# Performance work log

Hardware: AMD Instinct MI355X
Metric: run time of the kernel (lower is better)

## Reference

```python
import jax, jax.numpy as jnp
import numpy as np

B, L, E, H = 4, 2048, 1024, 16
D = E // H  # per-head dim

def setup_inputs() -> dict:
    key = jax.random.key(0)
    ks = jax.random.split(key, 12)
    xav = lambda k, shape: jax.random.normal(k, shape, jnp.float32) * (2.0 / (shape[0] + shape[-1])) ** 0.5
    embeddings = jax.random.normal(ks[0], (B, L, E), jnp.float32)
    pre_proj_w = xav(ks[1], (E, E)); pre_proj_b = jnp.zeros((E,), jnp.float32)
    pre_sparse_w = xav(ks[2], (E, E)); pre_sparse_b = jnp.zeros((E,), jnp.float32)
    toeplitz_psfs = xav(ks[3], (H, 2 * L - 1, D))
    post_conv_w = xav(ks[4], (E, E)); post_conv_b = jnp.zeros((E,), jnp.float32)
    dens = 0.01
    num_nz = int(L * L * dens)
    idxs = jax.random.randint(ks[5], (num_nz, 2), 0, L)
    vals = jnp.abs(jax.random.normal(ks[6], (num_nz,), jnp.float32))
    sparse = jnp.zeros((L, L), jnp.float32).at[idxs[:, 0], idxs[:, 1]].add(vals)
    ln_gamma = jnp.ones((E,), jnp.float32); ln_beta = jnp.zeros((E,), jnp.float32)
    return {"embeddings": embeddings, "pre_proj_w": pre_proj_w, "pre_proj_b": pre_proj_b,
            "pre_sparse_w": pre_sparse_w, "pre_sparse_b": pre_sparse_b,
            "toeplitz_psfs": toeplitz_psfs, "post_conv_w": post_conv_w, "post_conv_b": post_conv_b,
            "sparse": sparse, "ln_gamma": ln_gamma, "ln_beta": ln_beta}

def reference(embeddings, pre_proj_w, pre_proj_b, pre_sparse_w, pre_sparse_b,
              toeplitz_psfs, post_conv_w, post_conv_b, sparse, ln_gamma, ln_beta):
    b, l, e = embeddings.shape
    h, two_l_m1, d = toeplitz_psfs.shape
    # causal PSF mask: first l taps kept, trailing l-1 zeroed (before softmax)
    psf_mask = jnp.concatenate([jnp.ones((l,)), jnp.zeros((l - 1,))])[None, :, None]
    psfs = jax.nn.softmax(toeplitz_psfs * psf_mask, axis=1)  # softmax over 2l-1 taps
    # pre-projection
    pre = jnp.einsum('ble,oe->blo', embeddings, pre_proj_w) + pre_proj_b
    # pad seq to 2l-1 and split heads: [b, h, 2l-1, d]
    padded = jnp.pad(pre, ((0, 0), (0, l - 1), (0, 0)))
    padded = padded.reshape(b, two_l_m1, h, d).transpose(0, 2, 1, 3)
    # 2D FFT convolution over (seq, per-head-dim)
    psf_fft = jnp.fft.fftn(psfs, axes=(1, 2))              # [h, 2l-1, d]
    emb_fft = jnp.fft.fftn(padded, axes=(2, 3))            # [b, h, 2l-1, d]
    conv = jnp.real(jnp.fft.ifftn(psf_fft[None] * emb_fft, axes=(2, 3)))[:, :, :l, :]
    conv = jax.nn.gelu(conv, approximate=False)
    conv = conv.transpose(0, 2, 1, 3).reshape(b, l, e)
    conv_emb = jnp.einsum('ble,oe->blo', conv, post_conv_w) + post_conv_b
    # sparse branch (causal lower-triangular mask)
    sparse_masked = sparse * jnp.tril(jnp.ones((l, l), sparse.dtype))
    pre_sparse = jnp.einsum('ble,oe->blo', pre, pre_sparse_w) + pre_sparse_b
    sparse_emb = jnp.einsum('ls,bse->ble', sparse_masked, pre_sparse)
    # residual + layernorm (dropout = identity at eval)
    x = conv_emb + sparse_emb + embeddings
    mu = jnp.mean(x, axis=-1, keepdims=True)
    var = jnp.mean(jnp.square(x - mu), axis=-1, keepdims=True)
    return (x - mu) * jax.lax.rsqrt(var + 1e-12) * ln_gamma + ln_beta
```

## Files before the change

kernel.cpp:

```cpp
#include <hip/hip_runtime.h>
#include <hip/hip_bf16.h>
#include <hip/hip_fp16.h>
#include <math.h>

#define B_ 4
#define L_ 2048
#define E_ 1024
#define H_ 16
#define D_ 64
#define NFFT 4096
#define CAP 128

typedef __hip_bfloat16 bf16;
typedef __attribute__((ext_vector_type(8))) short bf16x8;
typedef __attribute__((ext_vector_type(4))) float f32x4;
typedef __attribute__((ext_vector_type(2))) __fp16 f16x2;

typedef __attribute__((address_space(1))) const unsigned int gas_u32;
typedef __attribute__((address_space(3))) unsigned int las_u32;

__device__ __forceinline__ void gload_lds16(const void* g, void* l) {
    __builtin_amdgcn_global_load_lds((gas_u32*)g, (las_u32*)l, 16, 0, 0);
}

#define SL(i) ((i) + ((i) >> 4))
#define LDSN (NFFT + NFFT / 16)

__device__ __forceinline__ float bfu2f(unsigned short u) {
    return __uint_as_float(((unsigned)u) << 16);
}
__device__ __forceinline__ f16x2 pk2(float a, float b) {
    return __builtin_amdgcn_cvt_pkrtz(a, b);
}

__device__ __forceinline__ int drev64(int k) {
    return ((k & 3) << 4) | (k & 12) | ((k >> 4) & 3);
}

#define C1R 0.923879532511287f
#define C1I -0.382683432365090f
#define C2R 0.707106781186548f
#define C2I -0.707106781186548f
#define C3R 0.382683432365090f
#define C3I -0.923879532511287f

__device__ __forceinline__ void r4dif_w(float& x0r, float& x0i, float& x1r, float& x1i,
                                        float& x2r, float& x2i, float& x3r, float& x3i,
                                        float w1r, float w1i) {
    float a0r = x0r + x2r, a0i = x0i + x2i, a1r = x0r - x2r, a1i = x0i - x2i;
    float a2r = x1r + x3r, a2i = x1i + x3i, a3r = x1r - x3r, a3i = x1i - x3i;
    float y0r = a0r + a2r, y0i = a0i + a2i, y2r = a0r - a2r, y2i = a0i - a2i;
    float y1r = a1r + a3i, y1i = a1i - a3r, y3r = a1r - a3i, y3i = a1i + a3r;
    float w2r = w1r * w1r - w1i * w1i, w2i = 2.0f * w1r * w1i;
    float w3r = w2r * w1r - w2i * w1i, w3i = w2r * w1i + w2i * w1r;
    x0r = y0r; x0i = y0i;
    x1r = y1r * w1r - y1i * w1i; x1i = y1r * w1i + y1i * w1r;
    x2r = y2r * w2r - y2i * w2i; x2i = y2r * w2i + y2i * w2r;
    x3r = y3r * w3r - y3i * w3i; x3i = y3r * w3i + y3i * w3r;
}
__device__ __forceinline__ void r4dif_nt(float& x0r, float& x0i, float& x1r, float& x1i,
                                         float& x2r, float& x2i, float& x3r, float& x3i) {
    float a0r = x0r + x2r, a0i = x0i + x2i, a1r = x0r - x2r, a1i = x0i - x2i;
    float a2r = x1r + x3r, a2i = x1i + x3i, a3r = x1r - x3r, a3i = x1i - x3i;
    x0r = a0r + a2r; x0i = a0i + a2i;
    x2r = a0r - a2r; x2i = a0i - a2i;
    float y1r = a1r + a3i, y1i = a1i - a3r, y3r = a1r - a3i, y3i = a1i + a3r;
    x1r = y1r; x1i = y1i; x3r = y3r; x3i = y3i;
}
__device__ __forceinline__ void r4dit_w(float& x0r, float& x0i, float& x1r, float& x1i,
                                        float& x2r, float& x2i, float& x3r, float& x3i,
                                        float w1r, float w1i) {
    float w2r = w1r * w1r - w1i * w1i, w2i = 2.0f * w1r * w1i;
    float w3r = w2r * w1r - w2i * w1i, w3i = w2r * w1i + w2i * w1r;
    float z1r = x1r * w1r + x1i * w1i, z1i = x1i * w1r - x1r * w1i;
    float z2r = x2r * w2r + x2i * w2i, z2i = x2i * w2r - x2r * w2i;
    float z3r = x3r * w3r + x3i * w3i, z3i = x3i * w3r - x3r * w3i;
    float b0r = x0r + z2r, b0i = x0i + z2i, b1r = x0r - z2r, b1i = x0i - z2i;
    float b2r = z1r + z3r, b2i = z1i + z3i, b3r = z1r - z3r, b3i = z1i - z3i;
    x0r = b0r + b2r; x0i = b0i + b2i;
    x2r = b0r - b2r; x2i = b0i - b2i;
    x1r = b1r - b3i; x1i = b1i + b3r;
    x3r = b1r + b3i; x3i = b1i - b3r;
}
__device__ __forceinline__ void r4dit_nt(float& x0r, float& x0i, float& x1r, float& x1i,
                                         float& x2r, float& x2i, float& x3r, float& x3i) {
    float b0r = x0r + x2r, b0i = x0i + x2i, b1r = x0r - x2r, b1i = x0i - x2i;
    float b2r = x1r + x3r, b2i = x1i + x3i, b3r = x1r - x3r, b3i = x1i - x3i;
    x0r = b0r + b2r; x0i = b0i + b2i;
    x2r = b0r - b2r; x2i = b0i - b2i;
    x1r = b1r - b3i; x1i = b1i + b3r;
    x3r = b1r + b3i; x3i = b1i - b3r;
}

__device__ __forceinline__ void fftA_fwd(float* xr, float* xi, float wpr, float wpi) {
    r4dif_w(xr[0], xi[0], xr[4], xi[4], xr[8], xi[8], xr[12], xi[12], wpr, wpi);
    r4dif_w(xr[1], xi[1], xr[5], xi[5], xr[9], xi[9], xr[13], xi[13],
            wpr * C1R - wpi * C1I, wpr * C1I + wpi * C1R);
    r4dif_w(xr[2], xi[2], xr[6], xi[6], xr[10], xi[10], xr[14], xi[14],
            wpr * C2R - wpi * C2I, wpr * C2I + wpi * C2R);
    r4dif_w(xr[3], xi[3], xr[7], xi[7], xr[11], xi[11], xr[15], xi[15],
            wpr * C3R - wpi * C3I, wpr * C3I + wpi * C3R);
    float s2r = wpr * wpr - wpi * wpi, s2i = 2.0f * wpr * wpi;
    float w4r = s2r * s2r - s2i * s2i, w4i = 2.0f * s2r * s2i;
#pragma unroll
    for (int g = 0; g < 4; ++g)
        r4dif_w(xr[4 * g], xi[4 * g], xr[4 * g + 1], xi[4 * g + 1], xr[4 * g + 2],
                xi[4 * g + 2], xr[4 * g + 3], xi[4 * g + 3], w4r, w4i);
}
__device__ __forceinline__ void fftA_inv(float* xr, float* xi, float wpr, float wpi) {
    float s2r = wpr * wpr - wpi * wpi, s2i = 2.0f * wpr * wpi;
    float w4r = s2r * s2r - s2i * s2i, w4i = 2.0f * s2r * s2i;
#pragma unroll
    for (int g = 0; g < 4; ++g)
        r4dit_w(xr[4 * g], xi[4 * g], xr[4 * g + 1], xi[4 * g + 1], xr[4 * g + 2],
                xi[4 * g + 2], xr[4 * g + 3], xi[4 * g + 3], w4r, w4i);
    r4dit_w(xr[0], xi[0], xr[4], xi[4], xr[8], xi[8], xr[12], xi[12], wpr, wpi);
    r4dit_w(xr[1], xi[1], xr[5], xi[5], xr[9], xi[9], xr[13], xi[13],
            wpr * C1R - wpi * C1I, wpr * C1I + wpi * C1R);
    r4dit_w(xr[2], xi[2], xr[6], xi[6], xr[10], xi[10], xr[14], xi[14],
            wpr * C2R - wpi * C2I, wpr * C2I + wpi * C2R);
    r4dit_w(xr[3], xi[3], xr[7], xi[7], xr[11], xi[11], xr[15], xi[15],
            wpr * C3R - wpi * C3I, wpr * C3I + wpi * C3R);
}
__device__ __forceinline__ void fftB_fwd(float* xr, float* xi, float wor, float woi) {
    r4dif_w(xr[0], xi[0], xr[4], xi[4], xr[8], xi[8], xr[12], xi[12], wor, woi);
    r4dif_w(xr[1], xi[1], xr[5], xi[5], xr[9], xi[9], xr[13], xi[13],
            wor * C1R - woi * C1I, wor * C1I + woi * C1R);
    r4dif_w(xr[2], xi[2], xr[6], xi[6], xr[10], xi[10], xr[14], xi[14],
            wor * C2R - woi * C2I, wor * C2I + woi * C2R);
    r4dif_w(xr[3], xi[3], xr[7], xi[7], xr[11], xi[11], xr[15], xi[15],
            wor * C3R - woi * C3I, wor * C3I + woi * C3R);
    float s2r = wor * wor - woi * woi, s2i = 2.0f * wor * woi;
    float w4r = s2r * s2r - s2i * s2i, w4i = 2.0f * s2r * s2i;
#pragma unroll
    for (int g = 0; g < 4; ++g)
        r4dif_w(xr[4 * g], xi[4 * g], xr[4 * g + 1], xi[4 * g + 1], xr[4 * g + 2],
                xi[4 * g + 2], xr[4 * g + 3], xi[4 * g + 3], w4r, w4i);
}
__device__ __forceinline__ void fftB_inv(float* xr, float* xi, float wor, float woi) {
    float s2r = wor * wor - woi * woi, s2i = 2.0f * wor * woi;
    float w4r = s2r * s2r - s2i * s2i, w4i = 2.0f * s2r * s2i;
#pragma unroll
    for (int g = 0; g < 4; ++g)
        r4dit_w(xr[4 * g], xi[4 * g], xr[4 * g + 1], xi[4 * g + 1], xr[4 * g + 2],
                xi[4 * g + 2], xr[4 * g + 3], xi[4 * g + 3], w4r, w4i);
    r4dit_w(xr[0], xi[0], xr[4], xi[4], xr[8], xi[8], xr[12], xi[12], wor, woi);
    r4dit_w(xr[1], xi[1], xr[5], xi[5], xr[9], xi[9], xr[13], xi[13],
            wor * C1R - woi * C1I, wor * C1I + woi * C1R);
    r4dit_w(xr[2], xi[2], xr[6], xi[6], xr[10], xi[10], xr[14], xi[14],
            wor * C2R - woi * C2I, wor * C2I + woi * C2R);
    r4dit_w(xr[3], xi[3], xr[7], xi[7], xr[11], xi[11], xr[15], xi[15],
            wor * C3R - woi * C3I, wor * C3I + woi * C3R);
}
__device__ __forceinline__ void fftC_fwd(float* xr, float* xi) {
    r4dif_w(xr[0], xi[0], xr[4], xi[4], xr[8], xi[8], xr[12], xi[12], 1.0f, 0.0f);
    r4dif_w(xr[1], xi[1], xr[5], xi[5], xr[9], xi[9], xr[13], xi[13], C1R, C1I);
    r4dif_w(xr[2], xi[2], xr[6], xi[6], xr[10], xi[10], xr[14], xi[14], C2R, C2I);
    r4dif_w(xr[3], xi[3], xr[7], xi[7], xr[11], xi[11], xr[15], xi[15], C3R, C3I);
#pragma unroll
    for (int g = 0; g < 4; ++g)
        r4dif_nt(xr[4 * g], xi[4 * g], xr[4 * g + 1], xi[4 * g + 1], xr[4 * g + 2],
                 xi[4 * g + 2], xr[4 * g + 3], xi[4 * g + 3]);
}
__device__ __forceinline__ void fftC_inv(float* xr, float* xi) {
#pragma unroll
    for (int g = 0; g < 4; ++g)
        r4dit_nt(xr[4 * g], xi[4 * g], xr[4 * g + 1], xi[4 * g + 1], xr[4 * g + 2],
                 xi[4 * g + 2], xr[4 * g + 3], xi[4 * g + 3]);
    r4dit_w(xr[0], xi[0], xr[4], xi[4], xr[8], xi[8], xr[12], xi[12], 1.0f, 0.0f);
    r4dit_w(xr[1], xi[1], xr[5], xi[5], xr[9], xi[9], xr[13], xi[13], C1R, C1I);
    r4dit_w(xr[2], xi[2], xr[6], xi[6], xr[10], xi[10], xr[14], xi[14], C2R, C2I);
    r4dit_w(xr[3], xi[3], xr[7], xi[7], xr[11], xi[11], xr[15], xi[15], C3R, C3I);
}

template <int CONJ>
__device__ inline void fft64_rows(float* xr, float* xi, int tid,
                                  const float2* __restrict__ tw) {
    for (int st = 0; st < 3; ++st) {
        int q = 1 << (4 - 2 * st);
        __syncthreads();
        for (int it = 0; it < 4; ++it) {
            int w = tid + (it << 8);
            int lc = w & 63, bc = w >> 6;
            int p = bc & (q - 1);
            int basev = ((bc & ~(q - 1)) << 2) | p;
            int i0 = basev * 66 + lc, i1 = i0 + q * 66, i2 = i1 + q * 66, i3 = i2 + q * 66;
            float x0r = xr[i0], x0i = xi[i0], x1r = xr[i1], x1i = xi[i1];
            float x2r = xr[i2], x2i = xi[i2], x3r = xr[i3], x3i = xi[i3];
            float a0r = x0r + x2r, a0i = x0i + x2i;
            float a1r = x0r - x2r, a1i = x0i - x2i;
            float a2r = x1r + x3r, a2i = x1i + x3i;
            float a3r = x1r - x3r, a3i = x1i - x3i;
            float y0r = a0r + a2r, y0i = a0i + a2i;
            float y2r = a0r - a2r, y2i = a0i - a2i;
            float y1r, y1i, y3r, y3i;
            if (!CONJ) {
                y1r = a1r + a3i; y1i = a1i - a3r;
                y3r = a1r - a3i; y3i = a1i + a3r;
            } else {
                y1r = a1r - a3i; y1i = a1i + a3r;
                y3r = a1r + a3i; y3i = a1i - a3r;
            }
            int e = (p << (2 * st)) * 64;
            float2 w1 = tw[e];
            float w1x = w1.x, w1y = CONJ ? -w1.y : w1.y;
            float w2x = w1x * w1x - w1y * w1y, w2y = 2.0f * w1x * w1y;
            float w3x = w2x * w1x - w2y * w1y, w3y = w2x * w1y + w2y * w1x;
            xr[i0] = y0r; xi[i0] = y0i;
            xr[i1] = y1r * w1x - y1i * w1y; xi[i1] = y1r * w1y + y1i * w1x;
            xr[i2] = y2r * w2x - y2i * w2y; xi[i2] = y2r * w2y + y2i * w2x;
            xr[i3] = y3r * w3x - y3i * w3y; xi[i3] = y3r * w3y + y3i * w3x;
        }
    }
    __syncthreads();
}

__device__ inline void fft64_b(float* xr, float* xi, int tid,
                               const float2* __restrict__ tw) {
    for (int st = 0; st < 3; ++st) {
        int q = 1 << (4 - 2 * st);
        __syncthreads();
        for (int it = 0; it < 4; ++it) {
            int b = tid + (it << 8);
            int fc = b & 63;
            int bc = b >> 6;
            int p = bc & (q - 1);
            int basev = ((bc & ~(q - 1)) << 2) | p;
            int i0 = basev * 64 + fc, i1 = i0 + q * 64, i2 = i1 + q * 64, i3 = i2 + q * 64;
            float x0r = xr[i0], x0i = xi[i0], x1r = xr[i1], x1i = xi[i1];
            float x2r = xr[i2], x2i = xi[i2], x3r = xr[i3], x3i = xi[i3];
            float a0r = x0r + x2r, a0i = x0i + x2i;
            float a1r = x0r - x2r, a1i = x0i - x2i;
            float a2r = x1r + x3r, a2i = x1i + x3i;
            float a3r = x1r - x3r, a3i = x1i - x3i;
            float y0r = a0r + a2r, y0i = a0i + a2i;
            float y2r = a0r - a2r, y2i = a0i - a2i;
            float y1r = a1r + a3i, y1i = a1i - a3r;
            float y3r = a1r - a3i, y3i = a1i + a3r;
            int e = (p << (2 * st)) * 64;
            float2 w1 = tw[e];
            float w2x = w1.x * w1.x - w1.y * w1.y, w2y = 2.0f * w1.x * w1.y;
            float w3x = w2x * w1.x - w2y * w1.y, w3y = w2x * w1.y + w2y * w1.x;
            xr[i0] = y0r; xi[i0] = y0i;
            xr[i1] = y1r * w1.x - y1i * w1.y; xi[i1] = y1r * w1.y + y1i * w1.x;
            xr[i2] = y2r * w2x - y2i * w2y; xi[i2] = y2r * w2y + y2i * w2x;
            xr[i3] = y3r * w3x - y3i * w3y; xi[i3] = y3r * w3y + y3i * w3x;
        }
    }
    __syncthreads();
}

#define NB_TW 16
#define NB_CVT 8192
#define NB_CVTW 3072
#define NB_TF 512
#define NB_SP 2048
__global__ __launch_bounds__(256) void k_prologue(const float* __restrict__ emb,
                                                  const float* __restrict__ W1,
                                                  const float* __restrict__ W2,
                                                  const float* __restrict__ W3,
                                                  const float* __restrict__ psfs,
                                                  const float* __restrict__ Sp,
                                                  float2* __restrict__ tw,
                                                  bf16* __restrict__ embb,
                                                  bf16* __restrict__ Wb,
                                                  float* __restrict__ psfT,
                                                  int* __restrict__ nnz,
                                                  int* __restrict__ idxs,
                                                  float* __restrict__ vals) {
    __shared__ float tile[64][65];
    __shared__ int cnt;
    int tid = threadIdx.x;
    int blk = blockIdx.x;
    if (blk < NB_TW) {
        int k = blk * 256 + tid;
        float ang = -(float)k * (float)(M_PI / 2048.0);
        tw[k] = make_float2(cosf(ang), sinf(ang));
        return;
    }
    blk -= NB_TW;
    if (blk < NB_CVT) {
        int i = (blk * 256 + tid) * 4;
        float4 v = *(const float4*)(emb + i);
        bf16 tmp[4];
        tmp[0] = __float2bfloat16(v.x); tmp[1] = __float2bfloat16(v.y);
        tmp[2] = __float2bfloat16(v.z); tmp[3] = __float2bfloat16(v.w);
        *(ushort4*)(embb + i) = *(ushort4*)tmp;
        return;
    }
    blk -= NB_CVT;
    if (blk < NB_CVTW) {
        int w = blk >> 10;
        const float* src = (w == 0) ? W1 : (w == 1) ? W2 : W3;
        int i = ((blk & 1023) * 256 + tid) * 4;
        float4 v = *(const float4*)(src + i);
        bf16 tmp[4];
        tmp[0] = __float2bfloat16(v.x); tmp[1] = __float2bfloat16(v.y);
        tmp[2] = __float2bfloat16(v.z); tmp[3] = __float2bfloat16(v.w);
        *(ushort4*)(Wb + (size_t)w * E_ * E_ + i) = *(ushort4*)tmp;
        return;
    }
    blk -= NB_CVTW;
    if (blk < NB_TF) {
        int z = blk >> 5;
        int r0 = (blk & 31) * 64;
        const float* in = psfs + (size_t)z * (2 * L_ - 1) * D_;
        float* out = psfT + (size_t)z * D_ * L_;
        int tx4 = (tid & 15) * 4, ty = tid >> 4;
#pragma unroll
        for (int k = 0; k < 4; ++k) {
            int r = ty + 16 * k;
            float4 v = *(const float4*)&in[(size_t)(r0 + r) * D_ + tx4];
            tile[r][tx4 + 0] = v.x; tile[r][tx4 + 1] = v.y;
            tile[r][tx4 + 2] = v.z; tile[r][tx4 + 3] = v.w;
        }
        __syncthreads();
#pragma unroll
        for (int k = 0; k < 4; ++k) {
            int c = ty + 16 * k;
            float4 w;
            w.x = tile[tx4 + 0][c]; w.y = tile[tx4 + 1][c];
            w.z = tile[tx4 + 2][c]; w.w = tile[tx4 + 3][c];
            *(float4*)&out[(size_t)c * L_ + r0 + tx4] = w;
        }
        return;
    }
    blk -= NB_TF;
    {
        int l = blk;
        if (tid == 0) cnt = 0;
        __syncthreads();
        const float* row = Sp + (size_t)l * L_;
        for (int s = tid; s <= l; s += 256) {
            float v = row[s];
            if (v != 0.0f) {
                int slot = atomicAdd(&cnt, 1);
                if (slot < CAP) { idxs[l * CAP + slot] = s; vals[l * CAP + slot] = v; }
            }
        }
        __syncthreads();
        if (tid == 0) nnz[l] = min(cnt, CAP);
    }
}

__device__ __forceinline__ void gemm_body(void* smemraw, int flat, int nwgx,
                                          const bf16* __restrict__ A,
                                          const bf16* __restrict__ Wt,
                                          const float* __restrict__ bias,
                                          bf16* __restrict__ Cb,
                                          int nwg, int N, int K) {
    bf16* As = (bf16*)smemraw;
    bf16* Bs = As + 64 * 64;
    int tid = threadIdx.x;
    int lane = tid & 63, w = tid >> 6;
    int wr = w >> 1, wc = w & 1;

    int cpx = nwg >> 3;
    int swz = (flat & 7) * cpx + (flat >> 3);
    int bx = (swz % nwgx) * 128;
    int by = (swz / nwgx) * 64;

    f32x4 zz = {0.0f, 0.0f, 0.0f, 0.0f};
    f32x4 acc[2][4];
#pragma unroll
    for (int m = 0; m < 2; ++m)
#pragma unroll
        for (int n = 0; n < 4; ++n) acc[m][n] = zz;

    int koff = (lane >> 4) * 8;
    int rsub = lane & 15;

    for (int k0 = 0; k0 < K; k0 += 64) {
#pragma unroll
        for (int i = 0; i < 2; ++i) {
            int c = tid + i * 256;
            int row = c >> 3;
            int kb = (c & 7) * 8;
            int kbs = kb ^ ((row & 7) << 3);
            gload_lds16(A + (size_t)(by + row) * K + k0 + kbs, &As[c * 8]);
        }
#pragma unroll
        for (int i = 0; i < 4; ++i) {
            int c = tid + i * 256;
            int row = c >> 3;
            int kb = (c & 7) * 8;
            int kbs = kb ^ ((row & 7) << 3);
            gload_lds16(Wt + (size_t)(bx + row) * K + k0 + kbs, &Bs[c * 8]);
        }
        __syncthreads();
#pragma unroll
        for (int half = 0; half < 2; ++half) {
            int ko = koff + half * 32;
            bf16x8 af[2], bfv[4];
#pragma unroll
            for (int m = 0; m < 2; ++m) {
                int R = wr * 32 + m * 16 + rsub;
                af[m] = *(const bf16x8*)&As[R * 64 + (ko ^ ((R & 7) << 3))];
            }
#pragma unroll
            for (int n = 0; n < 4; ++n) {
                int R = wc * 64 + n * 16 + rsub;
                bfv[n] = *(const bf16x8*)&Bs[R * 64 + (ko ^ ((R & 7) << 3))];
            }
#pragma unroll
            for (int m = 0; m < 2; ++m)
#pragma unroll
                for (int n = 0; n < 4; ++n)
                    acc[m][n] = __builtin_amdgcn_mfma_f32_16x16x32_bf16(af[m], bfv[n], acc[m][n], 0, 0, 0);
        }
        __syncthreads();
    }

    int cq = (lane >> 4) * 4;
    int cr = lane & 15;
#pragma unroll
    for (int m = 0; m < 2; ++m) {
        int row0 = by + wr * 32 + m * 16 + cq;
#pragma unroll
        for (int n = 0; n < 4; ++n) {
            int col = bx + wc * 64 + n * 16 + cr;
            float bv = bias[col];
#pragma unroll
            for (int j = 0; j < 4; ++j) {
                float v = acc[m][n][j] + bv;
                Cb[(size_t)(row0 + j) * N + col] = __float2bfloat16(v);
            }
        }
    }
}

__device__ __forceinline__ void khat_body(void* smemraw, int blk,
                                          const float* __restrict__ psfT,
                                          f16x2* __restrict__ Khat,
                                          const float2* __restrict__ tw) {
    f16x2* fl = (f16x2*)smemraw;
    float* red = (float*)(fl + LDSN);
    int u = blk & 63, h = blk >> 6;
    int tid = threadIdx.x;
    const float* col = psfT + ((size_t)(h * D_ + u)) * L_;
    int p = tid;

    float2 twp = tw[p];
    float2 two = tw[(tid & 15) * 16];

    float v[8];
#pragma unroll
    for (int j = 0; j < 8; ++j) v[j] = col[p + 256 * j];

    float lm = v[0];
#pragma unroll
    for (int j = 1; j < 8; ++j) lm = fmaxf(lm, v[j]);
    red[tid] = lm; __syncthreads();
    for (int off = 128; off > 0; off >>= 1) {
        if (tid < off) red[tid] = fmaxf(red[tid], red[tid + off]);
        __syncthreads();
    }
    float M = fmaxf(red[0], 0.0f);
    __syncthreads();

    float e[8];
    float ls = 0.0f;
#pragma unroll
    for (int j = 0; j < 8; ++j) { e[j] = expf(v[j] - M); ls += e[j]; }
    red[tid] = ls; __syncthreads();
    for (int off = 128; off > 0; off >>= 1) {
        if (tid < off) red[tid] += red[tid + off];
        __syncthreads();
    }
    float Z = red[0] + (float)(L_ - 1) * expf(-M);
    float invZ = 1.0f / Z;
    float cval = expf(-M) * invZ;

    float xr[16], xi[16];
#pragma unroll
    for (int j = 0; j < 16; ++j) {
        int i = p + 256 * j;
        xr[j] = (j < 8) ? e[j] * invZ : ((i == 2048) ? 0.0f : cval);
        xi[j] = 0.0f;
    }
    __syncthreads();

    fftA_fwd(xr, xi, twp.x, twp.y);
#pragma unroll
    for (int j = 0; j < 16; ++j) fl[SL(p + 256 * j)] = pk2(xr[j], xi[j]);
    __syncthreads();
    {
        int bb = tid >> 4, o = tid & 15;
#pragma unroll
        for (int j = 0; j < 16; ++j) {
            f16x2 hh = fl[SL(bb * 256 + o + 16 * j)];
            xr[j] = (float)hh.x; xi[j] = (float)hh.y;
        }
        fftB_fwd(xr, xi, two.x, two.y);
#pragma unroll
        for (int j = 0; j < 16; ++j)
            fl[SL(bb * 256 + o + 16 * j)] = pk2(xr[j], xi[j]);
    }
    __syncthreads();
#pragma unroll
    for (int j = 0; j < 16; ++j) {
        f16x2 hh = fl[SL(16 * tid + j)];
        xr[j] = (float)hh.x; xi[j] = (float)hh.y;
    }
    fftC_fwd(xr, xi);

    float sc = 1.0f / (float)NFFT;
    f16x2* outp = Khat + ((size_t)h * D_ + u) * NFFT + 16 * tid;
#pragma unroll
    for (int j = 0; j < 16; ++j) outp[j] = pk2(xr[j] * sc, xi[j] * sc);
}

__device__ __forceinline__ void dfft_body(void* smemraw, int blk,
                                          f16x2* __restrict__ Khat,
                                          const float2* __restrict__ tw) {
    float* Xre = (float*)smemraw;
    float* Xim = Xre + 4224;
    int tid = threadIdx.x;
    int f0 = (blk & 63) * 64, h = blk >> 6;
    f16x2* kb = Khat + (size_t)h * D_ * NFFT;
    for (int i = tid; i < 4096; i += 256) {
        int uu = i >> 6, fc = i & 63;
        f16x2 v = kb[(size_t)uu * NFFT + f0 + fc];
        Xre[i] = (float)v.x; Xim[i] = (float)v.y;
    }
    fft64_b(Xre, Xim, tid, tw);
    float sc = 1.0f / 64.0f;
    for (int i = tid; i < 4096; i += 256) {
        int s = i >> 6, fc = i & 63;
        kb[(size_t)drev64(s) * NFFT + f0 + fc] = pk2(Xre[i] * sc, Xim[i] * sc);
    }
}

__device__ __forceinline__ void vfft_body(void* smemraw, int blk,
                                          const bf16* __restrict__ preb,
                                          f16x2* __restrict__ Xv,
                                          const float2* __restrict__ tw) {
    float* Xre = (float*)smemraw;
    float* Xim = Xre + 4224;
    int tid = threadIdx.x;
    int l0 = (blk & 31) * 64, h = (blk >> 5) & 15, b = blk >> 9;
    const bf16* src = preb + ((size_t)(b * L_ + l0)) * E_ + h * 64;
#pragma unroll
    for (int it = 0; it < 2; ++it) {
        int c = tid + it * 256;
        int lc = c >> 3, v8 = (c & 7) * 8;
        bf16x8 xv8 = *(const bf16x8*)(src + (size_t)lc * E_ + v8);
#pragma unroll
        for (int j = 0; j < 8; ++j) {
            Xre[(v8 + j) * 66 + lc] = bfu2f((unsigned short)xv8[j]);
            Xim[(v8 + j) * 66 + lc] = 0.0f;
        }
    }
    fft64_rows<0>(Xre, Xim, tid, tw);
    for (int i = tid; i < 33 * 64; i += 256) {
        int k = i >> 6, lc = i & 63;
        int s = drev64(k);
        Xv[((size_t)(b * H_ + h) * 33 + k) * L_ + l0 + lc] =
            pk2(Xre[s * 66 + lc], Xim[s * 66 + lc]);
    }
}

__global__ __launch_bounds__(256) void k_gemm1_khat(const bf16* __restrict__ A,
                                                    const bf16* __restrict__ Wt,
                                                    const float* __restrict__ bias,
                                                    bf16* __restrict__ Cb,
                                                    const float* __restrict__ psfT,
                                                    f16x2* __restrict__ Khat,
                                                    const float2* __restrict__ tw) {
    __shared__ __align__(16) char smem[24576];
    int blk = blockIdx.x;
    if (blk < 1024)
        gemm_body(smem, blk, 8, A, Wt, bias, Cb, 1024, E_, E_);
    else
        khat_body(smem, blk - 1024, psfT, Khat, tw);
}

__global__ __launch_bounds__(256) void k_gemm2_dfft_vfft(const bf16* __restrict__ A,
                                                         const bf16* __restrict__ Wt,
                                                         const float* __restrict__ bias,
                                                         bf16* __restrict__ Cb,
                                                         f16x2* __restrict__ Khat,
                                                         f16x2* __restrict__ Xv,
                                                         const float2* __restrict__ tw) {
    __shared__ __align__(16) char smem[33792];
    int blk = blockIdx.x;
    if (blk < 1024)
        gemm_body(smem, blk, 8, A, Wt, bias, Cb, 1024, E_, E_);
    else if (blk < 2048)
        dfft_body(smem, blk - 1024, Khat, tw);
    else
        vfft_body(smem, blk - 2048, A, Xv, tw);
}

__global__ __launch_bounds__(256) void k_gemm3(const bf16* __restrict__ A,
                                               const bf16* __restrict__ Wt,
                                               const float* __restrict__ bias,
                                               bf16* __restrict__ Cb) {
    __shared__ __align__(16) char smem[24576];
    gemm_body(smem, blockIdx.x, 8, A, Wt, bias, Cb, 1024, E_, E_);
}

__global__ __launch_bounds__(256) void k_seqconv(f16x2* __restrict__ Xv,
                                                 const f16x2* __restrict__ Khat,
                                                 const float2* __restrict__ tw) {
    __shared__ f16x2 fl[LDSN];
    int k = blockIdx.x, h = blockIdx.y, b = blockIdx.z;
    int tid = threadIdx.x, p = tid;
    f16x2* col = Xv + ((size_t)(b * H_ + h) * 33 + k) * L_;

    float2 twp = tw[p];
    float2 two = tw[(tid & 15) * 16];

    float xr[16], xi[16];
#pragma unroll
    for (int j = 0; j < 16; ++j) {
        if (j < 8) {
            f16x2 z = col[p + 256 * j];
            xr[j] = (float)z.x; xi[j] = (float)z.y;
        } else { xr[j] = 0.0f; xi[j] = 0.0f; }
    }
    fftA_fwd(xr, xi, twp.x, twp.y);
#pragma unroll
    for (int j = 0; j < 16; ++j) fl[SL(p + 256 * j)] = pk2(xr[j], xi[j]);
    __syncthreads();
    {
        int bb = tid >> 4, o = tid & 15;
#pragma unroll
        for (int j = 0; j < 16; ++j) {
            f16x2 hh = fl[SL(bb * 256 + o + 16 * j)];
            xr[j] = (float)hh.x; xi[j] = (float)hh.y;
        }
        fftB_fwd(xr, xi, two.x, two.y);
#pragma unroll
        for (int j = 0; j < 16; ++j)
            fl[SL(bb * 256 + o + 16 * j)] = pk2(xr[j], xi[j]);
    }
    __syncthreads();
    {
        const f16x2* khp = Khat + ((size_t)h * 64 + k) * NFFT + 16 * tid;
        f16x2 kk[16];
#pragma unroll
        for (int j = 0; j < 16; ++j) kk[j] = khp[j];
#pragma unroll
        for (int j = 0; j < 16; ++j) {
            f16x2 hh = fl[SL(16 * tid + j)];
            xr[j] = (float)hh.x; xi[j] = (float)hh.y;
        }
        fftC_fwd(xr, xi);
#pragma unroll
        for (int j = 0; j < 16; ++j) {
            float kr = (float)kk[j].x, ki = (float)kk[j].y;
            float ar = xr[j], ai = xi[j];
            xr[j] = ar * kr - ai * ki;
            xi[j] = ar * ki + ai * kr;
        }
        fftC_inv(xr, xi);
#pragma unroll
        for (int j = 0; j < 16; ++j) fl[SL(16 * tid + j)] = pk2(xr[j], xi[j]);
    }
    __syncthreads();
    {
        int bb = tid >> 4, o = tid & 15;
#pragma unroll
        for (int j = 0; j < 16; ++j) {
            f16x2 hh = fl[SL(bb * 256 + o + 16 * j)];
            xr[j] = (float)hh.x; xi[j] = (float)hh.y;
        }
        fftB_inv(xr, xi, two.x, two.y);
#pragma unroll
        for (int j = 0; j < 16; ++j)
            fl[SL(bb * 256 + o + 16 * j)] = pk2(xr[j], xi[j]);
    }
    __syncthreads();
#pragma unroll
    for (int j = 0; j < 16; ++j) {
        f16x2 hh = fl[SL(p + 256 * j)];
        xr[j] = (float)hh.x; xi[j] = (float)hh.y;
    }
    fftA_inv(xr, xi, twp.x, twp.y);
#pragma unroll
    for (int j = 0; j < 8; ++j)
        col[p + 256 * j] = pk2(xr[j], xi[j]);
}

__global__ __launch_bounds__(256) void k_vifft(const f16x2* __restrict__ Xv,
                                               bf16* __restrict__ actb,
                                               const float2* __restrict__ tw) {
    __shared__ float Xre[64 * 66];
    __shared__ float Xim[64 * 66];
    int l0 = blockIdx.x * 64, h = blockIdx.y, b = blockIdx.z;
    int tid = threadIdx.x;
    for (int i = tid; i < 33 * 64; i += 256) {
        int k = i >> 6, lc = i & 63;
        f16x2 z = Xv[((size_t)(b * H_ + h) * 33 + k) * L_ + l0 + lc];
        Xre[k * 66 + lc] = (float)z.x; Xim[k * 66 + lc] = (float)z.y;
    }
    __syncthreads();
    for (int i = tid; i < 31 * 64; i += 256) {
        int k = 33 + (i >> 6), lc = i & 63;
        Xre[k * 66 + lc] =  Xre[(64 - k) * 66 + lc];
        Xim[k * 66 + lc] = -Xim[(64 - k) * 66 + lc];
    }
    fft64_rows<1>(Xre, Xim, tid, tw);
    bf16* dst = actb + ((size_t)(b * L_ + l0)) * E_ + h * 64;
#pragma unroll
    for (int it = 0; it < 2; ++it) {
        int c = tid + it * 256;
        int lc = c >> 3, m8 = (c & 7) * 8;
        unsigned short o[8];
#pragma unroll
        for (int j = 0; j < 8; ++j) {
            float x = Xre[drev64(m8 + j) * 66 + lc];
            float g = 0.5f * x * (1.0f + erff(x * 0.70710678118654752f));
            bf16 bb = __float2bfloat16(g);
            o[j] = *(unsigned short*)&bb;
        }
        *(ushort4*)(dst + (size_t)lc * E_ + m8)     = make_ushort4(o[0], o[1], o[2], o[3]);
        *(ushort4*)(dst + (size_t)lc * E_ + m8 + 4) = make_ushort4(o[4], o[5], o[6], o[7]);
    }
}

__global__ __launch_bounds__(256) void k_spmm_ln(const int* __restrict__ nnz,
                                                 const int* __restrict__ idxs,
                                                 const float* __restrict__ vals,
                                                 const bf16* __restrict__ P,
                                                 const bf16* __restrict__ accbb,
                                                 const float* __restrict__ emb,
                                                 const float* __restrict__ gamma,
                                                 const float* __restrict__ beta,
                                                 float* __restrict__ outp) {
    __shared__ int sidx[CAP];
    __shared__ float sval[CAP];
    __shared__ float red[256];
    int l = blockIdx.x, b = blockIdx.y, tid = threadIdx.x;
    int n = nnz[l];
    for (int j = tid; j < n; j += 256) {
        sidx[j] = idxs[l * CAP + j];
        sval[j] = vals[l * CAP + j];
    }
    __syncthreads();
    size_t off = (size_t)tid * 4;
    size_t rowbase = ((size_t)(b * L_ + l)) * E_;
    ushort4 a4 = *(const ushort4*)(accbb + rowbase + off);
    float4 e4 = *(const float4*)(emb + rowbase + off);
    float x0 = bfu2f(a4.x) + e4.x;
    float x1 = bfu2f(a4.y) + e4.y;
    float x2 = bfu2f(a4.z) + e4.z;
    float x3 = bfu2f(a4.w) + e4.w;
    const bf16* Pb = P + (size_t)b * L_ * E_;
    for (int j = 0; j < n; ++j) {
        float v = sval[j];
        ushort4 p = *(const ushort4*)(Pb + (size_t)sidx[j] * E_ + off);
        x0 += v * bfu2f(p.x); x1 += v * bfu2f(p.y);
        x2 += v * bfu2f(p.z); x3 += v * bfu2f(p.w);
    }
    red[tid] = x0 + x1 + x2 + x3; __syncthreads();
    for (int o2 = 128; o2 > 0; o2 >>= 1) {
        if (tid < o2) red[tid] += red[tid + o2];
        __syncthreads();
    }
    float mu = red[0] * (1.0f / E_);
    __syncthreads();
    float d0 = x0 - mu, d1 = x1 - mu, d2 = x2 - mu, d3 = x3 - mu;
    red[tid] = d0 * d0 + d1 * d1 + d2 * d2 + d3 * d3; __syncthreads();
    for (int o2 = 128; o2 > 0; o2 >>= 1) {
        if (tid < o2) red[tid] += red[tid + o2];
        __syncthreads();
    }
    float inv = rsqrtf(red[0] * (1.0f / E_) + 1e-12f);
    float4 g4 = *(const float4*)(gamma + off);
    float4 b4 = *(const float4*)(beta + off);
    float4 o4;
    o4.x = d0 * inv * g4.x + b4.x;
    o4.y = d1 * inv * g4.y + b4.y;
    o4.z = d2 * inv * g4.z + b4.z;
    o4.w = d3 * inv * g4.w + b4.w;
    *(float4*)(outp + rowbase + off) = o4;
}

extern "C" void kernel_launch(void* const* d_in, const int* in_sizes, int n_in,
                              void* d_out, int out_size, void* d_ws, size_t ws_size,
                              hipStream_t stream) {
    const float* emb    = (const float*)d_in[0];
    const float* W1     = (const float*)d_in[1];
    const float* b1     = (const float*)d_in[2];
    const float* W2     = (const float*)d_in[3];
    const float* b2     = (const float*)d_in[4];
    const float* psfs   = (const float*)d_in[5];
    const float* W3     = (const float*)d_in[6];
    const float* b3     = (const float*)d_in[7];
    const float* sparse = (const float*)d_in[8];
    const float* gamma  = (const float*)d_in[9];
    const float* beta   = (const float*)d_in[10];
    float* outp = (float*)d_out;

    const size_t BLE  = (size_t)B_ * L_ * E_;
    const size_t EE   = (size_t)E_ * E_;
    const size_t KSZ  = (size_t)H_ * D_ * NFFT;
    const size_t XVSZ = (size_t)B_ * H_ * 33 * L_;

    bf16*   accbb      = (bf16*)d_ws;
    bf16*   pre_sparse = accbb + BLE;
    f16x2*  Khat       = (f16x2*)(pre_sparse + BLE);
    f16x2*  Xv         = Khat + KSZ;
    bf16*   preb       = (bf16*)(Xv + XVSZ);
    bf16*   actb       = preb + BLE;
    bf16*   W1b        = actb + BLE;
    bf16*   W2b        = W1b + EE;
    bf16*   W3b        = W2b + EE;
    float2* twd        = (float2*)(W3b + EE);
    int*    s_nnz      = (int*)(twd + NFFT);
    int*    s_idx      = s_nnz + L_;
    float*  s_val      = (float*)(s_idx + (size_t)L_ * CAP);
    float*  psfT       = (float*)Xv;

    k_prologue<<<NB_TW + NB_CVT + NB_CVTW + NB_TF + NB_SP, 256, 0, stream>>>(
        emb, W1, W2, W3, psfs, sparse, twd, actb, W1b, psfT, s_nnz, s_idx, s_val);

    k_gemm1_khat<<<2048, 256, 0, stream>>>(actb, W1b, b1, preb, psfT, Khat, twd);

    k_gemm2_dfft_vfft<<<4096, 256, 0, stream>>>(preb, W2b, b2, pre_sparse, Khat, Xv, twd);

    k_seqconv<<<dim3(33, H_, B_), 256, 0, stream>>>(Xv, Khat, twd);

    k_vifft<<<dim3(L_ / 64, H_, B_), 256, 0, stream>>>(Xv, actb, twd);

    k_gemm3<<<1024, 256, 0, stream>>>(actb, W3b, b3, accbb);

    k_spmm_ln<<<dim3(L_, B_), 256, 0, stream>>>(
        s_nnz, s_idx, s_val, pre_sparse, accbb, emb, gamma, beta, outp);
}
```

Measured before the change: 197.0 us.

## Regroup fused launches: pair GEMM2 with sequence conv, interleave block types

```diff
diff --git a/kernel.cpp b/kernel.cpp
--- a/kernel.cpp
+++ b/kernel.cpp
@@ -560,6 +560,90 @@
     }
 }
 
+__device__ __forceinline__ void seq_body(void* smemraw, int sid,
+                                         f16x2* __restrict__ Xv,
+                                         const f16x2* __restrict__ Khat,
+                                         const float2* __restrict__ tw) {
+    f16x2* fl = (f16x2*)smemraw;
+    int k = sid % 33, h = (sid / 33) & 15, b = sid / 528;
+    int tid = threadIdx.x, p = tid;
+    f16x2* col = Xv + ((size_t)(b * H_ + h) * 33 + k) * L_;
+
+    float2 twp = tw[p];
+    float2 two = tw[(tid & 15) * 16];
+
+    float xr[16], xi[16];
+#pragma unroll
+    for (int j = 0; j < 16; ++j) {
+        if (j < 8) {
+            f16x2 z = col[p + 256 * j];
+            xr[j] = (float)z.x; xi[j] = (float)z.y;
+        } else { xr[j] = 0.0f; xi[j] = 0.0f; }
+    }
+    fftA_fwd(xr, xi, twp.x, twp.y);
+#pragma unroll
+    for (int j = 0; j < 16; ++j) fl[SL(p + 256 * j)] = pk2(xr[j], xi[j]);
+    __syncthreads();
+    {
+        int bb = tid >> 4, o = tid & 15;
+#pragma unroll
+        for (int j = 0; j < 16; ++j) {
+            f16x2 hh = fl[SL(bb * 256 + o + 16 * j)];
+            xr[j] = (float)hh.x; xi[j] = (float)hh.y;
+        }
+        fftB_fwd(xr, xi, two.x, two.y);
+#pragma unroll
+        for (int j = 0; j < 16; ++j)
+            fl[SL(bb * 256 + o + 16 * j)] = pk2(xr[j], xi[j]);
+    }
+    __syncthreads();
+    {
+        const f16x2* khp = Khat + ((size_t)h * 64 + k) * NFFT + 16 * tid;
+        f16x2 kk[16];
+#pragma unroll
+        for (int j = 0; j < 16; ++j) kk[j] = khp[j];
+#pragma unroll
+        for (int j = 0; j < 16; ++j) {
+            f16x2 hh = fl[SL(16 * tid + j)];
+            xr[j] = (float)hh.x; xi[j] = (float)hh.y;
+        }
+        fftC_fwd(xr, xi);
+#pragma unroll
+        for (int j = 0; j < 16; ++j) {
+            float kr = (float)kk[j].x, ki = (float)kk[j].y;
+            float ar = xr[j], ai = xi[j];
+            xr[j] = ar * kr - ai * ki;
+            xi[j] = ar * ki + ai * kr;
+        }
+        fftC_inv(xr, xi);
+#pragma unroll
+        for (int j = 0; j < 16; ++j) fl[SL(16 * tid + j)] = pk2(xr[j], xi[j]);
+    }
+    __syncthreads();
+    {
+        int bb = tid >> 4, o = tid & 15;
+#pragma unroll
+        for (int j = 0; j < 16; ++j) {
+            f16x2 hh = fl[SL(bb * 256 + o + 16 * j)];
+            xr[j] = (float)hh.x; xi[j] = (float)hh.y;
+        }
+        fftB_inv(xr, xi, two.x, two.y);
+#pragma unroll
+        for (int j = 0; j < 16; ++j)
+            fl[SL(bb * 256 + o + 16 * j)] = pk2(xr[j], xi[j]);
+    }
+    __syncthreads();
+#pragma unroll
+    for (int j = 0; j < 16; ++j) {
+        f16x2 hh = fl[SL(p + 256 * j)];
+        xr[j] = (float)hh.x; xi[j] = (float)hh.y;
+    }
+    fftA_inv(xr, xi, twp.x, twp.y);
+#pragma unroll
+    for (int j = 0; j < 8; ++j)
+        col[p + 256 * j] = pk2(xr[j], xi[j]);
+}
+
 __global__ __launch_bounds__(256) void k_gemm1_khat(const bf16* __restrict__ A,
                                                     const bf16* __restrict__ Wt,
                                                     const float* __restrict__ bias,
@@ -569,27 +653,39 @@
                                                     const float2* __restrict__ tw) {
     __shared__ __align__(16) char smem[24576];
     int blk = blockIdx.x;
-    if (blk < 1024)
-        gemm_body(smem, blk, 8, A, Wt, bias, Cb, 1024, E_, E_);
+    if ((blk & 1) == 0)
+        gemm_body(smem, blk >> 1, 8, A, Wt, bias, Cb, 1024, E_, E_);
     else
-        khat_body(smem, blk - 1024, psfT, Khat, tw);
-}
-
-__global__ __launch_bounds__(256) void k_gemm2_dfft_vfft(const bf16* __restrict__ A,
-                                                         const bf16* __restrict__ Wt,
-                                                         const float* __restrict__ bias,
-                                                         bf16* __restrict__ Cb,
-                                                         f16x2* __restrict__ Khat,
-                                                         f16x2* __restrict__ Xv,
-                                                         const float2* __restrict__ tw) {
+        khat_body(smem, blk >> 1, psfT, Khat, tw);
+}
+
+__global__ __launch_bounds__(256) void k_dfft_vfft(f16x2* __restrict__ Khat,
+                                                   const bf16* __restrict__ preb,
+                                                   f16x2* __restrict__ Xv,
+                                                   const float2* __restrict__ tw) {
     __shared__ __align__(16) char smem[33792];
     int blk = blockIdx.x;
     if (blk < 1024)
-        gemm_body(smem, blk, 8, A, Wt, bias, Cb, 1024, E_, E_);
-    else if (blk < 2048)
-        dfft_body(smem, blk - 1024, Khat, tw);
+        dfft_body(smem, blk, Khat, tw);
     else
-        vfft_body(smem, blk - 2048, A, Xv, tw);
+        vfft_body(smem, blk - 1024, preb, Xv, tw);
+}
+
+__global__ __launch_bounds__(256) void k_seq_gemm2(f16x2* __restrict__ Xv,
+                                                   const f16x2* __restrict__ Khat,
+                                                   const bf16* __restrict__ A,
+                                                   const bf16* __restrict__ Wt,
+                                                   const float* __restrict__ bias,
+                                                   bf16* __restrict__ Cb,
+                                                   const float2* __restrict__ tw) {
+    __shared__ __align__(16) char smem[24576];
+    int blk = blockIdx.x;
+    if (blk < 3072 && (blk % 3) == 2) {
+        gemm_body(smem, blk / 3, 8, A, Wt, bias, Cb, 1024, E_, E_);
+    } else {
+        int sid = (blk < 3072) ? blk - blk / 3 : blk - 1024;
+        seq_body(smem, sid, Xv, Khat, tw);
+    }
 }
 
 __global__ __launch_bounds__(256) void k_gemm3(const bf16* __restrict__ A,
@@ -598,89 +694,6 @@
                                                bf16* __restrict__ Cb) {
     __shared__ __align__(16) char smem[24576];
     gemm_body(smem, blockIdx.x, 8, A, Wt, bias, Cb, 1024, E_, E_);
-}
-
-__global__ __launch_bounds__(256) void k_seqconv(f16x2* __restrict__ Xv,
-                                                 const f16x2* __restrict__ Khat,
-                                                 const float2* __restrict__ tw) {
-    __shared__ f16x2 fl[LDSN];
-    int k = blockIdx.x, h = blockIdx.y, b = blockIdx.z;
-    int tid = threadIdx.x, p = tid;
-    f16x2* col = Xv + ((size_t)(b * H_ + h) * 33 + k) * L_;
-
-    float2 twp = tw[p];
-    float2 two = tw[(tid & 15) * 16];
-
-    float xr[16], xi[16];
-#pragma unroll
-    for (int j = 0; j < 16; ++j) {
-        if (j < 8) {
-            f16x2 z = col[p + 256 * j];
-            xr[j] = (float)z.x; xi[j] = (float)z.y;
-        } else { xr[j] = 0.0f; xi[j] = 0.0f; }
-    }
-    fftA_fwd(xr, xi, twp.x, twp.y);
-#pragma unroll
-    for (int j = 0; j < 16; ++j) fl[SL(p + 256 * j)] = pk2(xr[j], xi[j]);
-    __syncthreads();
-    {
-        int bb = tid >> 4, o = tid & 15;
-#pragma unroll
-        for (int j = 0; j < 16; ++j) {
-            f16x2 hh = fl[SL(bb * 256 + o + 16 * j)];
-            xr[j] = (float)hh.x; xi[j] = (float)hh.y;
-        }
-        fftB_fwd(xr, xi, two.x, two.y);
-#pragma unroll
-        for (int j = 0; j < 16; ++j)
-            fl[SL(bb * 256 + o + 16 * j)] = pk2(xr[j], xi[j]);
-    }
-    __syncthreads();
-    {
-        const f16x2* khp = Khat + ((size_t)h * 64 + k) * NFFT + 16 * tid;
-        f16x2 kk[16];
-#pragma unroll
-        for (int j = 0; j < 16; ++j) kk[j] = khp[j];
-#pragma unroll
-        for (int j = 0; j < 16; ++j) {
-            f16x2 hh = fl[SL(16 * tid + j)];
-            xr[j] = (float)hh.x; xi[j] = (float)hh.y;
-        }
-        fftC_fwd(xr, xi);
-#pragma unroll
-        for (int j = 0; j < 16; ++j) {
-            float kr = (float)kk[j].x, ki = (float)kk[j].y;
-            float ar = xr[j], ai = xi[j];
-            xr[j] = ar * kr - ai * ki;
-            xi[j] = ar * ki + ai * kr;
-        }
-        fftC_inv(xr, xi);
-#pragma unroll
-        for (int j = 0; j < 16; ++j) fl[SL(16 * tid + j)] = pk2(xr[j], xi[j]);
-    }
-    __syncthreads();
-    {
-        int bb = tid >> 4, o = tid & 15;
-#pragma unroll
-        for (int j = 0; j < 16; ++j) {
-            f16x2 hh = fl[SL(bb * 256 + o + 16 * j)];
-            xr[j] = (float)hh.x; xi[j] = (float)hh.y;
-        }
-        fftB_inv(xr, xi, two.x, two.y);
-#pragma unroll
-        for (int j = 0; j < 16; ++j)
-            fl[SL(bb * 256 + o + 16 * j)] = pk2(xr[j], xi[j]);
-    }
-    __syncthreads();
-#pragma unroll
-    for (int j = 0; j < 16; ++j) {
-        f16x2 hh = fl[SL(p + 256 * j)];
-        xr[j] = (float)hh.x; xi[j] = (float)hh.y;
-    }
-    fftA_inv(xr, xi, twp.x, twp.y);
-#pragma unroll
-    for (int j = 0; j < 8; ++j)
-        col[p + 256 * j] = pk2(xr[j], xi[j]);
 }
 
 __global__ __launch_bounds__(256) void k_vifft(const f16x2* __restrict__ Xv,
@@ -819,9 +832,9 @@
 
     k_gemm1_khat<<<2048, 256, 0, stream>>>(actb, W1b, b1, preb, psfT, Khat, twd);
 
-    k_gemm2_dfft_vfft<<<4096, 256, 0, stream>>>(preb, W2b, b2, pre_sparse, Khat, Xv, twd);
-
-    k_seqconv<<<dim3(33, H_, B_), 256, 0, stream>>>(Xv, Khat, twd);
+    k_dfft_vfft<<<3072, 256, 0, stream>>>(Khat, preb, Xv, twd);
+
+    k_seq_gemm2<<<3136, 256, 0, stream>>>(Xv, Khat, preb, W2b, b2, pre_sparse, twd);
 
     k_vifft<<<dim3(L_ / 64, H_, B_), 256, 0, stream>>>(Xv, actb, twd);
 
```

Result: slower. 213.5 us (+8.4%).
